# Optimization experiments

Hardware: AMD Instinct MI355X
Metric: run time of the kernel (lower is better)

Reference implementation:

```python
import jax, jax.numpy as jnp
import numpy as np

P = 8        # kernel_size (window size)
HEADS = 8
HC = 256     # hidden_channels
CIN = 256    # in_channels


def setup_inputs() -> dict:
    key = jax.random.key(0)
    ks = jax.random.split(key, 6)
    return {
        "x": jax.random.normal(ks[0], (4, CIN, 128, 128), jnp.float32),
        "w_qkv": jax.random.normal(ks[1], (3 * HC, CIN), jnp.float32) * (2.0 / CIN) ** 0.5,
        "b_qkv": jnp.zeros((3 * HC,), jnp.float32),
        "position": jax.random.normal(ks[2], (HC, P, P), jnp.float32) * 0.02,
        "w_out": jax.random.normal(ks[3], (CIN, HC), jnp.float32) * (2.0 / HC) ** 0.5,
        "b_out": jnp.zeros((CIN,), jnp.float32),
    }


def _windows(t, B, nH, nW):
    # [B, HC, Hp, Wp] -> [B, heads, nWin, P*P, dh]
    dh = HC // HEADS
    t = t.reshape(B, HEADS, dh, nH, P, nW, P)
    t = t.transpose(0, 1, 3, 5, 4, 6, 2)  # B, heads, nH, nW, P, P, dh
    return t.reshape(B, HEADS, nH * nW, P * P, dh)


def _forward(x, w_qkv, b_qkv, position, w_out, b_out):
    B, C, H, W = x.shape
    # NOTE: faithful to source - pad components are in [1, P], never zero
    pad_w, pad_h = P - W % P, P - H % P
    xp = jnp.pad(x, ((0, 0), (0, 0),
                     (pad_h // 2, pad_h - pad_h // 2),
                     (pad_w // 2, pad_w - pad_w // 2)))
    Hp, Wp = xp.shape[2], xp.shape[3]
    nH, nW = Hp // P, Wp // P
    dh = HC // HEADS
    # 1x1 conv qkv projection (pointwise GEMM)
    qkv = jnp.einsum('bchw,oc->bohw', xp, w_qkv) + b_qkv[None, :, None, None]
    q, k, v = jnp.split(qkv, 3, axis=1)
    q = _windows(q, B, nH, nW)
    k = _windows(k, B, nH, nW)
    v = _windows(v, B, nH, nW)
    # learned relative position bias, added to queries, shared across windows
    pos = position.reshape(HEADS, dh, P * P).transpose(0, 2, 1)  # heads, P*P, dh
    q = q + pos[None, :, None, :, :]
    scale = 1.0 / jnp.sqrt(jnp.asarray(dh, x.dtype))
    attn = jax.nn.softmax(jnp.einsum('bhnqd,bhnkd->bhnqk', q, k) * scale, axis=-1)
    o = jnp.einsum('bhnqk,bhnkd->bhnqd', attn, v)  # B, heads, nWin, P*P, dh
    o = o.reshape(B, HEADS, nH, nW, P, P, dh).transpose(0, 1, 6, 2, 4, 3, 5)
    o = o.reshape(B, HC, Hp, Wp)
    y = jnp.einsum('bchw,oc->bohw', o, w_out) + b_out[None, :, None, None]
    return y[:, :, pad_h // 2:H + pad_h // 2, pad_w // 2:W + pad_w // 2]


def reference(x, w_qkv, b_qkv, position, w_out, b_out):
    return _forward(x, w_qkv, b_qkv, position, w_out, b_out)
```

## Files before the change

kernel.cpp:

```cpp
#include <hip/hip_runtime.h>


typedef __attribute__((ext_vector_type(8))) short bf16x8;
typedef __attribute__((ext_vector_type(4))) float f32x4;

#define NWROW 17
#define NWIN  289
#define ATT_SCALE 0.17677669529663687f

#define XS_STRIDE 264
#define XS_SIZE   (64 * XS_STRIDE)
#define WPRIV     2560
#define LDS_USH   (XS_SIZE + 8 * WPRIV)

__device__ __forceinline__ ushort f2bf(float f) {
    unsigned u = __float_as_uint(f);
    u += 0x7FFFu + ((u >> 16) & 1u);
    return (ushort)(u >> 16);
}
__device__ __forceinline__ unsigned pack2(float a, float b) {
    return (unsigned)f2bf(a) | ((unsigned)f2bf(b) << 16);
}

__global__ void lsa_wconv(const float* __restrict__ wqkv,
                          const float* __restrict__ wout,
                          ushort* __restrict__ dst)
{
    int n = blockIdx.x * 256 + threadIdx.x;
    float v = (n < 196608) ? wqkv[n] : wout[n - 196608];
    dst[n] = f2bf(v);
}

__global__ __launch_bounds__(512, 4)
void lsa_fused(const float* __restrict__ x,
               const float* __restrict__ bqkv,
               const float* __restrict__ posb,
               const float* __restrict__ bout,
               const ushort* __restrict__ wqkvb,
               const ushort* __restrict__ woutb,
               float* __restrict__ y)
{
    __shared__ __align__(16) ushort sm[LDS_USH];

    const int t    = threadIdx.x;
    const int wv   = t >> 6;
    const int lane = t & 63;
    const int g    = lane >> 4;
    const int c    = lane & 15;
    const int head = wv;

    const int orig = blockIdx.x;
    const int xcd  = orig & 7;
    const int idx  = orig >> 3;
    const int bid  = (xcd < 4 ? xcd * 145 : 580 + (xcd - 4) * 144) + idx;

    const int b   = bid / NWIN;
    const int win = bid - b * NWIN;
    const int wi  = win / NWROW;
    const int wj  = win - wi * NWROW;
    const int hbase = wi * 8 - 4;
    const int wbase = wj * 8 - 4;

    #pragma unroll
    for (int i = 0; i < 8; ++i) {
        int id = (i << 9) + t;
        int ch = id >> 4;
        int qd = id & 15;
        int h  = hbase + (qd >> 1);
        int w0 = wbase + (qd & 1) * 4;
        f32x4 v = (f32x4){0.f, 0.f, 0.f, 0.f};
        if ((unsigned)h < 128u && (unsigned)w0 < 125u)
            v = *(const f32x4*)&x[(((size_t)b * 256 + ch) * 128 + h) * 128 + w0];
        ushort bs[4] = {f2bf(v[0]), f2bf(v[1]), f2bf(v[2]), f2bf(v[3])};
        #pragma unroll
        for (int e = 0; e < 4; ++e) {
            int ee = (e + qd) & 3;
            sm[(qd * 4 + ee) * XS_STRIDE + ch] = bs[ee];
        }
    }
    __syncthreads();

    ushort* priv = &sm[XS_SIZE + wv * WPRIV];

    f32x4 acc[4][4];
    #pragma unroll
    for (int i = 0; i < 4; ++i)
        #pragma unroll
        for (int j = 0; j < 4; ++j)
            acc[i][j] = (f32x4){0.f, 0.f, 0.f, 0.f};

    const ushort* wr[4];
    #pragma unroll
    for (int j = 0; j < 4; ++j) {
        int m0 = (j >> 1) * 256 + head * 32 + (j & 1) * 16;
        wr[j] = wqkvb + (size_t)(m0 + c) * 256;
    }

    #pragma unroll
    for (int ks = 0; ks < 8; ++ks) {
        bf16x8 bfr[4];
        #pragma unroll
        for (int pt = 0; pt < 4; ++pt)
            bfr[pt] = *(const bf16x8*)&sm[(pt * 16 + c) * XS_STRIDE + ks * 32 + 8 * g];
        #pragma unroll
        for (int j = 0; j < 4; ++j) {
            bf16x8 afr = *(const bf16x8*)(wr[j] + ks * 32 + 8 * g);
            #pragma unroll
            for (int pt = 0; pt < 4; ++pt)
                acc[j][pt] = __builtin_amdgcn_mfma_f32_16x16x32_bf16(afr, bfr[pt], acc[j][pt], 0, 0, 0);
        }
    }

    #pragma unroll
    for (int mt = 0; mt < 2; ++mt) {
        f32x4 bq = *(const f32x4*)&bqkv[head * 32 + mt * 16 + 4 * g];
        #pragma unroll
        for (int pt = 0; pt < 4; ++pt) {
            const int pos = pt * 16 + c;
            const float* pb = posb + (size_t)(head * 32 + mt * 16 + 4 * g) * 64 + pos;
            float v0 = (acc[mt][pt][0] + bq[0] + pb[0])   * ATT_SCALE;
            float v1 = (acc[mt][pt][1] + bq[1] + pb[64])  * ATT_SCALE;
            float v2 = (acc[mt][pt][2] + bq[2] + pb[128]) * ATT_SCALE;
            float v3 = (acc[mt][pt][3] + bq[3] + pb[192]) * ATT_SCALE;
            *(unsigned*)&priv[pos * 40 + mt * 16 + 4 * g]     = pack2(v0, v1);
            *(unsigned*)&priv[pos * 40 + mt * 16 + 4 * g + 2] = pack2(v2, v3);
        }
    }
    bf16x8 qf[4];
    #pragma unroll
    for (int qt = 0; qt < 4; ++qt)
        qf[qt] = *(const bf16x8*)&priv[(qt * 16 + c) * 40 + 8 * g];

    #pragma unroll
    for (int mt = 0; mt < 2; ++mt) {
        f32x4 bk = *(const f32x4*)&bqkv[256 + head * 32 + mt * 16 + 4 * g];
        #pragma unroll
        for (int pt = 0; pt < 4; ++pt) {
            const int pos = pt * 16 + c;
            *(unsigned*)&priv[pos * 40 + mt * 16 + 4 * g]     = pack2(acc[mt + 2][pt][0] + bk[0], acc[mt + 2][pt][1] + bk[1]);
            *(unsigned*)&priv[pos * 40 + mt * 16 + 4 * g + 2] = pack2(acc[mt + 2][pt][2] + bk[2], acc[mt + 2][pt][3] + bk[3]);
        }
    }
    bf16x8 kf[4];
    #pragma unroll
    for (int kt = 0; kt < 4; ++kt)
        kf[kt] = *(const bf16x8*)&priv[(kt * 16 + c) * 40 + 8 * g];

    f32x4 av[2][4];
    #pragma unroll
    for (int i = 0; i < 2; ++i)
        #pragma unroll
        for (int j = 0; j < 4; ++j)
            av[i][j] = (f32x4){0.f, 0.f, 0.f, 0.f};
    const ushort* wv0 = wqkvb + (size_t)(512 + head * 32 + c) * 256;
    const ushort* wv1 = wqkvb + (size_t)(512 + head * 32 + 16 + c) * 256;

    #pragma unroll
    for (int ks = 0; ks < 8; ++ks) {
        bf16x8 bfr[4];
        #pragma unroll
        for (int pt = 0; pt < 4; ++pt)
            bfr[pt] = *(const bf16x8*)&sm[(pt * 16 + c) * XS_STRIDE + ks * 32 + 8 * g];
        bf16x8 a0 = *(const bf16x8*)(wv0 + ks * 32 + 8 * g);
        bf16x8 a1 = *(const bf16x8*)(wv1 + ks * 32 + 8 * g);
        #pragma unroll
        for (int pt = 0; pt < 4; ++pt) {
            av[0][pt] = __builtin_amdgcn_mfma_f32_16x16x32_bf16(a0, bfr[pt], av[0][pt], 0, 0, 0);
            av[1][pt] = __builtin_amdgcn_mfma_f32_16x16x32_bf16(a1, bfr[pt], av[1][pt], 0, 0, 0);
        }
    }

    #pragma unroll
    for (int mt = 0; mt < 2; ++mt) {
        f32x4 bv = *(const f32x4*)&bqkv[512 + head * 32 + mt * 16 + 4 * g];
        #pragma unroll
        for (int pt = 0; pt < 4; ++pt) {
            #pragma unroll
            for (int r = 0; r < 4; ++r)
                priv[(mt * 16 + 4 * g + r) * 72 + pt * 16 + c] = f2bf(av[mt][pt][r] + bv[r]);
        }
    }

    f32x4 s[4][4];
    #pragma unroll
    for (int kt = 0; kt < 4; ++kt)
        #pragma unroll
        for (int qt = 0; qt < 4; ++qt)
            s[kt][qt] = __builtin_amdgcn_mfma_f32_16x16x32_bf16(kf[kt], qf[qt],
                                                                (f32x4){0.f,0.f,0.f,0.f}, 0, 0, 0);

    float rinv[4];
    #pragma unroll
    for (int qt = 0; qt < 4; ++qt) {
        float mx = s[0][qt][0];
        #pragma unroll
        for (int kt = 0; kt < 4; ++kt)
            #pragma unroll
            for (int r = 0; r < 4; ++r)
                mx = fmaxf(mx, s[kt][qt][r]);
        mx = fmaxf(mx, __shfl_xor(mx, 16));
        mx = fmaxf(mx, __shfl_xor(mx, 32));
        float sum = 0.f;
        #pragma unroll
        for (int kt = 0; kt < 4; ++kt)
            #pragma unroll
            for (int r = 0; r < 4; ++r) {
                s[kt][qt][r] = __expf(s[kt][qt][r] - mx);
                sum += s[kt][qt][r];
            }
        sum += __shfl_xor(sum, 16);
        sum += __shfl_xor(sum, 32);
        rinv[qt] = 1.0f / sum;
    }

    bf16x8 vf[2][2];
    #pragma unroll
    for (int dt = 0; dt < 2; ++dt)
        #pragma unroll
        for (int k2 = 0; k2 < 2; ++k2)
            vf[dt][k2] = *(const bf16x8*)&priv[(dt * 16 + c) * 72 + k2 * 32 + 8 * g];

    f32x4 o[2][4];
    #pragma unroll
    for (int dt = 0; dt < 2; ++dt)
        #pragma unroll
        for (int qt = 0; qt < 4; ++qt)
            o[dt][qt] = (f32x4){0.f,0.f,0.f,0.f};

    #pragma unroll
    for (int k2 = 0; k2 < 2; ++k2) {
        #pragma unroll
        for (int qt = 0; qt < 4; ++qt)
            #pragma unroll
            for (int kl = 0; kl < 2; ++kl) {
                const int kt = k2 * 2 + kl;
                *(unsigned*)&priv[(qt * 16 + c) * 40 + kl * 16 + 4 * g]     = pack2(s[kt][qt][0], s[kt][qt][1]);
                *(unsigned*)&priv[(qt * 16 + c) * 40 + kl * 16 + 4 * g + 2] = pack2(s[kt][qt][2], s[kt][qt][3]);
            }
        #pragma unroll
        for (int qt = 0; qt < 4; ++qt) {
            bf16x8 pf = *(const bf16x8*)&priv[(qt * 16 + c) * 40 + 8 * g];
            #pragma unroll
            for (int dt = 0; dt < 2; ++dt)
                o[dt][qt] = __builtin_amdgcn_mfma_f32_16x16x32_bf16(vf[dt][k2], pf, o[dt][qt], 0, 0, 0);
        }
    }

    __syncthreads();

    #pragma unroll
    for (int dt = 0; dt < 2; ++dt)
        #pragma unroll
        for (int qt = 0; qt < 4; ++qt) {
            const int pos = qt * 16 + c;
            const int ch0 = head * 32 + dt * 16 + 4 * g;
            float rv = rinv[qt];
            *(unsigned*)&sm[pos * XS_STRIDE + ch0]     = pack2(o[dt][qt][0]*rv, o[dt][qt][1]*rv);
            *(unsigned*)&sm[pos * XS_STRIDE + ch0 + 2] = pack2(o[dt][qt][2]*rv, o[dt][qt][3]*rv);
        }
    __syncthreads();

    f32x4 ya[2][4];
    #pragma unroll
    for (int i = 0; i < 2; ++i)
        #pragma unroll
        for (int j = 0; j < 4; ++j)
            ya[i][j] = (f32x4){0.f,0.f,0.f,0.f};

    const ushort* wo0 = woutb + (size_t)(wv * 32 + c) * 256;
    const ushort* wo1 = woutb + (size_t)(wv * 32 + 16 + c) * 256;

    #pragma unroll
    for (int ks = 0; ks < 8; ++ks) {
        bf16x8 ofr[4];
        #pragma unroll
        for (int pt = 0; pt < 4; ++pt)
            ofr[pt] = *(const bf16x8*)&sm[(pt * 16 + c) * XS_STRIDE + ks * 32 + 8 * g];
        bf16x8 a0 = *(const bf16x8*)(wo0 + ks * 32 + 8 * g);
        bf16x8 a1 = *(const bf16x8*)(wo1 + ks * 32 + 8 * g);
        #pragma unroll
        for (int pt = 0; pt < 4; ++pt) {
            ya[0][pt] = __builtin_amdgcn_mfma_f32_16x16x32_bf16(a0, ofr[pt], ya[0][pt], 0, 0, 0);
            ya[1][pt] = __builtin_amdgcn_mfma_f32_16x16x32_bf16(a1, ofr[pt], ya[1][pt], 0, 0, 0);
        }
    }

    float* ysp = (float*)priv;
    #pragma unroll
    for (int mt = 0; mt < 2; ++mt) {
        f32x4 bo = *(const f32x4*)&bout[wv * 32 + mt * 16 + 4 * g];
        #pragma unroll
        for (int pt = 0; pt < 4; ++pt) {
            const int pos = pt * 16 + c;
            #pragma unroll
            for (int r = 0; r < 4; ++r)
                ysp[(4 * g + r) * 66 + pos] = ya[mt][pt][r] + bo[r];
        }
        #pragma unroll
        for (int k = 0; k < 2; ++k) {
            const int cl = k * 8 + (lane >> 3);
            const int hh = lane & 7;
            float2 p0 = *(float2*)&ysp[cl * 66 + hh * 8];
            float2 p1 = *(float2*)&ysp[cl * 66 + hh * 8 + 2];
            float2 p2 = *(float2*)&ysp[cl * 66 + hh * 8 + 4];
            float2 p3 = *(float2*)&ysp[cl * 66 + hh * 8 + 6];
            const int co  = wv * 32 + mt * 16 + cl;
            const int him = wi * 8 + hh - 4;
            if ((unsigned)him < 128u) {
                float* yrow = y + (((size_t)b * 256 + co) * 128 + him) * 128;
                if (wj > 0)  { f32x4 v0 = {p0.x, p0.y, p1.x, p1.y}; *(f32x4*)&yrow[wbase]     = v0; }
                if (wj < 16) { f32x4 v1 = {p2.x, p2.y, p3.x, p3.y}; *(f32x4*)&yrow[wbase + 4] = v1; }
            }
        }
    }
}

extern "C" void kernel_launch(void* const* d_in, const int* in_sizes, int n_in,
                              void* d_out, int out_size, void* d_ws, size_t ws_size,
                              hipStream_t stream)
{
    const float* x    = (const float*)d_in[0];
    const float* wqkv = (const float*)d_in[1];
    const float* bqkv = (const float*)d_in[2];
    const float* posb = (const float*)d_in[3];
    const float* wout = (const float*)d_in[4];
    const float* bout = (const float*)d_in[5];
    float* y = (float*)d_out;

    ushort* wqkvb = (ushort*)d_ws;
    ushort* woutb = wqkvb + 196608;

    lsa_wconv<<<dim3(1024), dim3(256), 0, stream>>>(wqkv, wout, wqkvb);
    lsa_fused<<<dim3(4 * NWIN), dim3(512), 0, stream>>>(x, bqkv, posb, bout, wqkvb, woutb, y);
}
```

Measured before the change: 125.9 us.

## Split fused window attention kernel into attention and output-projection kernels

Measured after the change: 151.0 us. 19.9% more time.

```diff
diff --git a/kernel.cpp b/kernel.cpp
--- a/kernel.cpp
+++ b/kernel.cpp
@@ -20,6 +20,10 @@
 }
 __device__ __forceinline__ unsigned pack2(float a, float b) {
     return (unsigned)f2bf(a) | ((unsigned)f2bf(b) << 16);
+}
+__device__ __forceinline__ int xcd_swz(int orig) {
+    int xcd = orig & 7, idx = orig >> 3;
+    return (xcd < 4 ? xcd * 145 : 580 + (xcd - 4) * 144) + idx;
 }
 
 __global__ void lsa_wconv(const float* __restrict__ wqkv,
@@ -32,13 +36,11 @@
 }
 
 __global__ __launch_bounds__(512, 4)
-void lsa_fused(const float* __restrict__ x,
-               const float* __restrict__ bqkv,
-               const float* __restrict__ posb,
-               const float* __restrict__ bout,
-               const ushort* __restrict__ wqkvb,
-               const ushort* __restrict__ woutb,
-               float* __restrict__ y)
+void lsa_qkattn(const float* __restrict__ x,
+                const float* __restrict__ bqkv,
+                const float* __restrict__ posb,
+                const ushort* __restrict__ wqkvb,
+                ushort* __restrict__ ows)
 {
     __shared__ __align__(16) ushort sm[LDS_USH];
 
@@ -49,11 +51,7 @@
     const int c    = lane & 15;
     const int head = wv;
 
-    const int orig = blockIdx.x;
-    const int xcd  = orig & 7;
-    const int idx  = orig >> 3;
-    const int bid  = (xcd < 4 ? xcd * 145 : 580 + (xcd - 4) * 144) + idx;
-
+    const int bid = xcd_swz(blockIdx.x);
     const int b   = bid / NWIN;
     const int win = bid - b * NWIN;
     const int wi  = win / NWROW;
@@ -246,8 +244,7 @@
         }
     }
 
-    __syncthreads();
-
+    ushort* ow = ows + (size_t)(b * NWIN + win) * 16384;
     #pragma unroll
     for (int dt = 0; dt < 2; ++dt)
         #pragma unroll
@@ -255,40 +252,75 @@
             const int pos = qt * 16 + c;
             const int ch0 = head * 32 + dt * 16 + 4 * g;
             float rv = rinv[qt];
-            *(unsigned*)&sm[pos * XS_STRIDE + ch0]     = pack2(o[dt][qt][0]*rv, o[dt][qt][1]*rv);
-            *(unsigned*)&sm[pos * XS_STRIDE + ch0 + 2] = pack2(o[dt][qt][2]*rv, o[dt][qt][3]*rv);
-        }
+            *(uint2*)&ow[pos * 256 + ch0] =
+                make_uint2(pack2(o[dt][qt][0]*rv, o[dt][qt][1]*rv),
+                           pack2(o[dt][qt][2]*rv, o[dt][qt][3]*rv));
+        }
+}
+
+__global__ __launch_bounds__(256, 4)
+void lsa_out(const ushort* __restrict__ ows,
+             const ushort* __restrict__ woutb,
+             const float* __restrict__ bout,
+             float* __restrict__ y)
+{
+    __shared__ __align__(16) ushort os[64 * XS_STRIDE];
+
+    const int t    = threadIdx.x;
+    const int wv   = t >> 6;
+    const int lane = t & 63;
+    const int g    = lane >> 4;
+    const int c    = lane & 15;
+
+    const int bid = xcd_swz(blockIdx.x);
+    const int b   = bid / NWIN;
+    const int win = bid - b * NWIN;
+    const int wi  = win / NWROW;
+    const int wj  = win - wi * NWROW;
+    const int wbase = wj * 8 - 4;
+
+    const ushort* src = ows + (size_t)(b * NWIN + win) * 16384;
+    #pragma unroll
+    for (int j = 0; j < 8; ++j) {
+        int chunk = j * 256 + t;
+        int pos = chunk >> 5;
+        int ch0 = (chunk & 31) * 8;
+        *(bf16x8*)&os[pos * XS_STRIDE + ch0] = *(const bf16x8*)&src[chunk * 8];
+    }
     __syncthreads();
 
-    f32x4 ya[2][4];
-    #pragma unroll
-    for (int i = 0; i < 2; ++i)
+    f32x4 ya[4][4];
+    #pragma unroll
+    for (int i = 0; i < 4; ++i)
         #pragma unroll
         for (int j = 0; j < 4; ++j)
             ya[i][j] = (f32x4){0.f,0.f,0.f,0.f};
 
-    const ushort* wo0 = woutb + (size_t)(wv * 32 + c) * 256;
-    const ushort* wo1 = woutb + (size_t)(wv * 32 + 16 + c) * 256;
+    const ushort* wo[4];
+    #pragma unroll
+    for (int mt = 0; mt < 4; ++mt)
+        wo[mt] = woutb + (size_t)(wv * 64 + mt * 16 + c) * 256;
 
     #pragma unroll
     for (int ks = 0; ks < 8; ++ks) {
         bf16x8 ofr[4];
         #pragma unroll
         for (int pt = 0; pt < 4; ++pt)
-            ofr[pt] = *(const bf16x8*)&sm[(pt * 16 + c) * XS_STRIDE + ks * 32 + 8 * g];
-        bf16x8 a0 = *(const bf16x8*)(wo0 + ks * 32 + 8 * g);
-        bf16x8 a1 = *(const bf16x8*)(wo1 + ks * 32 + 8 * g);
-        #pragma unroll
-        for (int pt = 0; pt < 4; ++pt) {
-            ya[0][pt] = __builtin_amdgcn_mfma_f32_16x16x32_bf16(a0, ofr[pt], ya[0][pt], 0, 0, 0);
-            ya[1][pt] = __builtin_amdgcn_mfma_f32_16x16x32_bf16(a1, ofr[pt], ya[1][pt], 0, 0, 0);
-        }
-    }
-
-    float* ysp = (float*)priv;
-    #pragma unroll
-    for (int mt = 0; mt < 2; ++mt) {
-        f32x4 bo = *(const f32x4*)&bout[wv * 32 + mt * 16 + 4 * g];
+            ofr[pt] = *(const bf16x8*)&os[(pt * 16 + c) * XS_STRIDE + ks * 32 + 8 * g];
+        #pragma unroll
+        for (int mt = 0; mt < 4; ++mt) {
+            bf16x8 afr = *(const bf16x8*)(wo[mt] + ks * 32 + 8 * g);
+            #pragma unroll
+            for (int pt = 0; pt < 4; ++pt)
+                ya[mt][pt] = __builtin_amdgcn_mfma_f32_16x16x32_bf16(afr, ofr[pt], ya[mt][pt], 0, 0, 0);
+        }
+    }
+    __syncthreads();
+
+    float* ysp = (float*)&os[wv * 2112];
+    #pragma unroll
+    for (int mt = 0; mt < 4; ++mt) {
+        f32x4 bo = *(const f32x4*)&bout[wv * 64 + mt * 16 + 4 * g];
         #pragma unroll
         for (int pt = 0; pt < 4; ++pt) {
             const int pos = pt * 16 + c;
@@ -304,7 +336,7 @@
             float2 p1 = *(float2*)&ysp[cl * 66 + hh * 8 + 2];
             float2 p2 = *(float2*)&ysp[cl * 66 + hh * 8 + 4];
             float2 p3 = *(float2*)&ysp[cl * 66 + hh * 8 + 6];
-            const int co  = wv * 32 + mt * 16 + cl;
+            const int co  = wv * 64 + mt * 16 + cl;
             const int him = wi * 8 + hh - 4;
             if ((unsigned)him < 128u) {
                 float* yrow = y + (((size_t)b * 256 + co) * 128 + him) * 128;
@@ -329,7 +361,9 @@
 
     ushort* wqkvb = (ushort*)d_ws;
     ushort* woutb = wqkvb + 196608;
+    ushort* ows   = wqkvb + 262144;
 
     lsa_wconv<<<dim3(1024), dim3(256), 0, stream>>>(wqkv, wout, wqkvb);
-    lsa_fused<<<dim3(4 * NWIN), dim3(512), 0, stream>>>(x, bqkv, posb, bout, wqkvb, woutb, y);
-}
+    lsa_qkattn<<<dim3(4 * NWIN), dim3(512), 0, stream>>>(x, bqkv, posb, wqkvb, ows);
+    lsa_out<<<dim3(4 * NWIN), dim3(256), 0, stream>>>(ows, woutb, bout, y);
+}
```
